# Kernel tuning notes

Measured on AMD Instinct MI355X. Metric: run time of the kernel, lower is better.

The kernel has to match this reference:

```python
import jax, jax.numpy as jnp
import numpy as np

DECAY = 0.99
EPS = 1e-05
B, C, H, W = 64, 64, 64, 64   # C == embedding_dim
K = 512                       # num_embedding


def setup_inputs() -> dict:
    key = jax.random.key(0)
    k1, k2 = jax.random.split(key)
    inp = jax.random.normal(k1, (B, C, H, W), dtype=jnp.float32)
    embedding = jax.random.normal(k2, (C, K), dtype=jnp.float32)
    cluster_size = jnp.zeros((K,), dtype=jnp.float32)
    embedding_avg = embedding  # buffer initialized as a clone of embedding
    return {"input": inp, "embedding": embedding,
            "cluster_size": cluster_size, "embedding_avg": embedding_avg}


def reference(input, embedding, cluster_size, embedding_avg):
    # NCHW -> NHWC, flatten to [N, C]
    x = jnp.transpose(input, (0, 2, 3, 1))           # [B,H,W,C]
    flat = x.reshape(-1, embedding.shape[0])          # [N,C]
    # squared L2 distances to all K codes: [N,K]
    dist = (jnp.sum(flat * flat, axis=1, keepdims=True)
            - 2.0 * flat @ embedding
            + jnp.sum(embedding * embedding, axis=0, keepdims=True))
    ind = jnp.argmin(dist, axis=1)                    # [N] int
    # gather codes (uses OLD embedding, as in torch)
    quantize = jnp.take(embedding.T, ind, axis=0).reshape(x.shape)  # [B,H,W,C]
    # EMA updates (training branch). Avoid materializing one-hot:
    counts = jnp.zeros((K,), dtype=flat.dtype).at[ind].add(1.0)      # onehot.sum(0)
    embedding_sum = jax.ops.segment_sum(flat, ind, num_segments=K).T  # [C,K] == flat.T @ onehot
    new_cluster_size = cluster_size * DECAY + (1.0 - DECAY) * counts
    new_embedding_avg = embedding_avg * DECAY + (1.0 - DECAY) * embedding_sum
    n = jnp.sum(new_cluster_size)
    cs = (new_cluster_size + EPS) / (n + K * EPS) * n
    new_embedding = new_embedding_avg / cs[None, :]
    # commitment loss and straight-through estimator
    diff = jnp.mean((jax.lax.stop_gradient(quantize) - x) ** 2)
    quantize_st = x + jax.lax.stop_gradient(quantize - x)
    out = jnp.transpose(quantize_st, (0, 3, 1, 2))    # back to NCHW
    embedding_ind = ind.reshape(x.shape[:-1])         # [B,H,W]
    return out, diff, embedding_ind, new_embedding, new_cluster_size, new_embedding_avg
```

## Files before the change

### kernel.cpp

```cpp
#include <hip/hip_runtime.h>
#include <cstdint>
#include <cstddef>

typedef _Float16 half4v __attribute__((ext_vector_type(4)));
typedef _Float16 half8v __attribute__((ext_vector_type(8)));
typedef float    f32x4  __attribute__((ext_vector_type(4)));

#define N_PTS   262144
#define CDIM    64
#define KCODES  512
#define TAUA    5e-3f
#define FLAG_CAP 65536u

#define OFF_DIFF 16777216u
#define OFF_IND  16777217u
#define OFF_EMB  17039361u
#define OFF_CSZ  17072129u
#define OFF_AVG  17072641u

__global__ __launch_bounds__(512) void k_main(
    const float* __restrict__ in, const float* __restrict__ emb,
    float* __restrict__ out,
    int* __restrict__ ind_buf, float* __restrict__ diff_acc,
    unsigned* __restrict__ nflag, int* __restrict__ flaglist)
{
    __shared__ __align__(16) char bsm[133120];
    float* ee2_lds = (float*)(bsm + 131072);
    const int tid = threadIdx.x;

    {
        const int col = tid;
        const int xr  = (col & 7) << 4;
        float s = 0.f;
        #pragma unroll
        for (int c0 = 0; c0 < CDIM; c0 += 4) {
            float v[4];
            #pragma unroll
            for (int i = 0; i < 4; ++i) v[i] = emb[(c0 + i)*KCODES + col];
            half4v h, lo;
            #pragma unroll
            for (int i = 0; i < 4; ++i) {
                s = fmaf(v[i], v[i], s);
                _Float16 hh = (_Float16)v[i];
                h[i]  = hh;
                lo[i] = (_Float16)(v[i] - (float)hh);
            }
            const int wb = col*128 + ((c0*2) ^ xr);
            *(half4v*)(bsm + wb)         = h;
            *(half4v*)(bsm + 65536 + wb) = lo;
        }
        ee2_lds[col] = 0.5f * s;
    }
    __syncthreads();

    const int w  = tid >> 6, l = tid & 63;
    const int g  = l >> 4,  lc = l & 15;

    for (int r = 0; r < 2; ++r) {
        const int pbase = (blockIdx.x << 10) + (r << 9) + (w << 6);
        const int b     = pbase >> 12;
        const float* inb = in + ((size_t)b << 18) + ((pbase & 4095) + lc);

        half8v ah[4][2], al[4][2];
        float xs = 0.f;
        #pragma unroll
        for (int t = 0; t < 4; ++t)
            #pragma unroll
            for (int s = 0; s < 2; ++s)
                #pragma unroll
                for (int j = 0; j < 8; ++j) {
                    const int c = s*32 + g*8 + j;
                    const float x = inb[(size_t)c*4096 + t*16];
                    xs = fmaf(x, x, xs);
                    const float xf = -x;
                    const _Float16 hh = (_Float16)xf;
                    ah[t][s][j] = hh;
                    al[t][s][j] = (_Float16)(xf - (float)hh);
                }

        float d1[4][4], d2[4][4]; int k1[4][4];
        #pragma unroll
        for (int t = 0; t < 4; ++t)
            #pragma unroll
            for (int rr = 0; rr < 4; ++rr) { d1[t][rr] = 3.4e38f; d2[t][rr] = 3.4e38f; k1[t][rr] = 0; }

        for (int ct = 0; ct < 32; ++ct) {
            const int col  = (ct << 4) + lc;
            const float sd = ee2_lds[col];
            const int rb   = col*128 + ((g*16) ^ ((col & 7) << 4));
            half8v bh0 = *(const half8v*)(bsm + rb);
            half8v bh1 = *(const half8v*)(bsm + (rb ^ 64));
            half8v bl0 = *(const half8v*)(bsm + 65536 + rb);
            half8v bl1 = *(const half8v*)(bsm + 65536 + (rb ^ 64));

            #pragma unroll
            for (int t = 0; t < 4; ++t) {
                f32x4 acc = {sd, sd, sd, sd};
                acc = __builtin_amdgcn_mfma_f32_16x16x32_f16(al[t][0], bh0, acc, 0, 0, 0);
                acc = __builtin_amdgcn_mfma_f32_16x16x32_f16(al[t][1], bh1, acc, 0, 0, 0);
                acc = __builtin_amdgcn_mfma_f32_16x16x32_f16(ah[t][0], bl0, acc, 0, 0, 0);
                acc = __builtin_amdgcn_mfma_f32_16x16x32_f16(ah[t][1], bl1, acc, 0, 0, 0);
                acc = __builtin_amdgcn_mfma_f32_16x16x32_f16(ah[t][0], bh0, acc, 0, 0, 0);
                acc = __builtin_amdgcn_mfma_f32_16x16x32_f16(ah[t][1], bh1, acc, 0, 0, 0);
                #pragma unroll
                for (int rr = 0; rr < 4; ++rr) {
                    const float d = acc[rr];
                    const bool cc = d < d1[t][rr];
                    d2[t][rr] = fminf(d2[t][rr], fmaxf(d, d1[t][rr]));
                    d1[t][rr] = fminf(d1[t][rr], d);
                    k1[t][rr] = cc ? col : k1[t][rr];
                }
            }
        }

        #pragma unroll
        for (int m = 1; m <= 8; m <<= 1) {
            #pragma unroll
            for (int t = 0; t < 4; ++t)
                #pragma unroll
                for (int rr = 0; rr < 4; ++rr) {
                    const float od1 = __shfl_xor(d1[t][rr], m);
                    const int   ok1 = __shfl_xor(k1[t][rr], m);
                    const float od2 = __shfl_xor(d2[t][rr], m);
                    const float nd2 = fminf(fmaxf(d1[t][rr], od1), fminf(d2[t][rr], od2));
                    const bool take = (od1 < d1[t][rr]) || (od1 == d1[t][rr] && ok1 < k1[t][rr]);
                    d1[t][rr] = take ? od1 : d1[t][rr];
                    k1[t][rr] = take ? ok1 : k1[t][rr];
                    d2[t][rr] = nd2;
                }
        }

        float ds = 0.f;
        if (lc == 0) {
            #pragma unroll
            for (int t = 0; t < 4; ++t) {
                const int nb = pbase + t*16 + (g << 2);
                int4 iv = make_int4(k1[t][0], k1[t][1], k1[t][2], k1[t][3]);
                *(int4*)(ind_buf + nb) = iv;
                #pragma unroll
                for (int rr = 0; rr < 4; ++rr) {
                    out[OFF_IND + nb + rr] = (float)k1[t][rr];
                    ds += d1[t][rr];
                    if (d2[t][rr] - d1[t][rr] < TAUA) {
                        unsigned ix = atomicAdd(nflag, 1u);
                        if (ix < FLAG_CAP) flaglist[ix] = nb + rr;
                    }
                }
            }
        }
        #pragma unroll
        for (int m = 1; m < 64; m <<= 1) {
            ds += __shfl_xor(ds, m);
            xs += __shfl_xor(xs, m);
        }
        if (l == 0) atomicAdd(diff_acc, 2.f*ds + xs);
    }
}

__global__ void k_refine(const float* __restrict__ in, const float* __restrict__ emb,
                         const unsigned* __restrict__ nflag, const int* __restrict__ flaglist,
                         int* __restrict__ ind_buf, float* __restrict__ out)
{
    const int gtid = blockIdx.x*blockDim.x + threadIdx.x;
    const int wid  = gtid >> 6;
    const int lane = threadIdx.x & 63;
    const int nw   = (gridDim.x * blockDim.x) >> 6;
    unsigned nf = *nflag; if (nf > FLAG_CAP) nf = FLAG_CAP;
    for (unsigned f = wid; f < nf; f += nw) {
        const int n = flaglist[f];
        const int b = n >> 12, hw = n & 4095;
        const float* xb = in + ((size_t)b << 18) + hw;
        const float* er = emb + lane*8;
        double dd[8] = {0,0,0,0,0,0,0,0};
        for (int c = 0; c < CDIM; ++c) {
            const double xv = (double)xb[(size_t)c << 12];
            #pragma unroll
            for (int j = 0; j < 8; ++j) {
                double t = xv - (double)er[c*KCODES + j];
                dd[j] = fma(t, t, dd[j]);
            }
        }
        double bd = 1e300; int bk = 0;
        #pragma unroll
        for (int j = 0; j < 8; ++j) {
            const int kk = lane*8 + j;
            if (dd[j] < bd) { bd = dd[j]; bk = kk; }
        }
        for (int off = 32; off; off >>= 1) {
            double od = __shfl_xor(bd, off);
            int    ok = __shfl_xor(bk, off);
            if (od < bd || (od == bd && ok < bk)) { bd = od; bk = ok; }
        }
        if (lane == 0) { ind_buf[n] = bk; out[OFF_IND + n] = (float)bk; }
    }
}

__global__ __launch_bounds__(512) void k_stats(const float* __restrict__ in,
    const int* __restrict__ ind_buf, float* __restrict__ p_sum, float* __restrict__ p_cnt)
{
    __shared__ __align__(16) char xsm[2][CDIM*128];
    __shared__ int   ind_lds[2][32];
    __shared__ float s_cnt[KCODES];

    const int tid = threadIdx.x;
    const int wg  = blockIdx.x;
    const int n0  = wg << 10;
    const int b   = n0 >> 12;
    const float* inb = in + ((size_t)b << 18) + (n0 & 4095);

    for (int i = tid; i < KCODES; i += 512) s_cnt[i] = 0.f;

    const int sc  = tid >> 3;
    const int sp  = (tid & 7) << 2;
    const int sxr = (sc & 7) << 4;
    const int wb_hi = sc*128 + ((sp*2)      ^ sxr);
    const int wb_lo = sc*128 + ((64 + sp*2) ^ sxr);

    const int w  = tid >> 6, l = tid & 63;
    const int g  = l >> 4,  lc = l & 15;
    const int k0w = w << 6;

    f32x4 acc[4][4];
    #pragma unroll
    for (int ci = 0; ci < 4; ++ci)
        #pragma unroll
        for (int kt = 0; kt < 4; ++kt) acc[ci][kt] = (f32x4){0.f, 0.f, 0.f, 0.f};

    {
        const float4 xv = *(const float4*)(inb + (size_t)sc*4096 + sp);
        half4v h, lo;
        #pragma unroll
        for (int i = 0; i < 4; ++i) {
            const float x = ((const float*)&xv)[i];
            _Float16 hh = (_Float16)x;
            h[i] = hh; lo[i] = (_Float16)(x - (float)hh);
        }
        *(half4v*)(&xsm[0][0] + wb_hi) = h;
        *(half4v*)(&xsm[0][0] + wb_lo) = lo;
        if (tid < 8) *(int4*)&ind_lds[0][tid*4] = *(const int4*)(ind_buf + n0 + tid*4);
    }

    for (int t = 0; t < 32; ++t) {
        __syncthreads();
        float4 nxt; int4 niv;
        if (t < 31) {
            nxt = *(const float4*)(inb + (size_t)sc*4096 + (t+1)*32 + sp);
            if (tid < 8) niv = *(const int4*)(ind_buf + n0 + (t+1)*32 + tid*4);
        }
        if (tid < 32) atomicAdd(&s_cnt[ind_lds[t & 1][tid]], 1.f);

        const char* xb = &xsm[t & 1][0];
        half8v ah[4], al[4];
        #pragma unroll
        for (int ci = 0; ci < 4; ++ci) {
            const int c  = (ci << 4) + lc;
            const int xr = (c & 7) << 4;
            ah[ci] = *(const half8v*)(xb + c*128 + ((g*16)      ^ xr));
            al[ci] = *(const half8v*)(xb + c*128 + ((64 + g*16) ^ xr));
        }
        int idv[8];
        *(int4*)&idv[0] = *(const int4*)&ind_lds[t & 1][g*8];
        *(int4*)&idv[4] = *(const int4*)&ind_lds[t & 1][g*8 + 4];
        #pragma unroll
        for (int kt = 0; kt < 4; ++kt) {
            const int tgt = k0w + (kt << 4) + lc;
            half8v bf;
            #pragma unroll
            for (int j = 0; j < 8; ++j) bf[j] = (idv[j] == tgt) ? (_Float16)1.0f : (_Float16)0.0f;
            #pragma unroll
            for (int ci = 0; ci < 4; ++ci) {
                acc[ci][kt] = __builtin_amdgcn_mfma_f32_16x16x32_f16(ah[ci], bf, acc[ci][kt], 0, 0, 0);
                acc[ci][kt] = __builtin_amdgcn_mfma_f32_16x16x32_f16(al[ci], bf, acc[ci][kt], 0, 0, 0);
            }
        }
        if (t < 31) {
            half4v h, lo;
            #pragma unroll
            for (int i = 0; i < 4; ++i) {
                const float x = ((const float*)&nxt)[i];
                _Float16 hh = (_Float16)x;
                h[i] = hh; lo[i] = (_Float16)(x - (float)hh);
            }
            char* xn = &xsm[(t+1) & 1][0];
            *(half4v*)(xn + wb_hi) = h;
            *(half4v*)(xn + wb_lo) = lo;
            if (tid < 8) *(int4*)&ind_lds[(t+1) & 1][tid*4] = niv;
        }
    }
    __syncthreads();

    float* ps = p_sum + (size_t)wg * (CDIM*KCODES);
    #pragma unroll
    for (int ci = 0; ci < 4; ++ci)
        #pragma unroll
        for (int kt = 0; kt < 4; ++kt)
            #pragma unroll
            for (int rr = 0; rr < 4; ++rr)
                ps[((ci << 4) + (g << 2) + rr)*KCODES + k0w + (kt << 4) + lc] = acc[ci][kt][rr];
    float* pc = p_cnt + wg * KCODES;
    for (int i = tid; i < KCODES; i += 512) pc[i] = s_cnt[i];
}

__global__ __launch_bounds__(256) void k_reduce1(const float* __restrict__ p_sum,
    const float* __restrict__ p_cnt, float* __restrict__ partial8,
    float* __restrict__ cnt8, int wsl)
{
    const int ic = blockIdx.x & 31, ws = blockIdx.x >> 5;
    const int i4 = ic*1024 + threadIdx.x*4;
    const float* base = p_sum + (size_t)ws*wsl*(CDIM*KCODES) + i4;
    float4 s = make_float4(0.f, 0.f, 0.f, 0.f);
    for (int w = 0; w < wsl; ++w) {
        const float4 v = *(const float4*)(base + (size_t)w*(CDIM*KCODES));
        s.x += v.x; s.y += v.y; s.z += v.z; s.w += v.w;
    }
    *(float4*)(partial8 + ws*(CDIM*KCODES) + i4) = s;
    if (ic == 0) {
        for (int k = threadIdx.x; k < KCODES; k += 256) {
            float c = 0.f;
            for (int w = 0; w < wsl; ++w) c += p_cnt[(ws*wsl + w)*KCODES + k];
            cnt8[ws*KCODES + k] = c;
        }
    }
}

__global__ __launch_bounds__(256) void k_reduce2(const float* __restrict__ partial8,
    const float* __restrict__ cnt8, float* __restrict__ sum_tot, float* __restrict__ cnt_tot)
{
    const int i4 = (blockIdx.x*256 + threadIdx.x)*4;
    float4 s = make_float4(0.f, 0.f, 0.f, 0.f);
    #pragma unroll
    for (int p = 0; p < 8; ++p) {
        const float4 v = *(const float4*)(partial8 + p*(CDIM*KCODES) + i4);
        s.x += v.x; s.y += v.y; s.z += v.z; s.w += v.w;
    }
    *(float4*)(sum_tot + i4) = s;
    if (blockIdx.x == 0) {
        for (int k = threadIdx.x; k < KCODES; k += 256) {
            float c = 0.f;
            #pragma unroll
            for (int p = 0; p < 8; ++p) c += cnt8[p*KCODES + k];
            cnt_tot[k] = c;
        }
    }
}

__global__ __launch_bounds__(512) void k_scalars(const float* __restrict__ csz,
    const float* __restrict__ cnt_tot, const float* __restrict__ diff_acc,
    float* __restrict__ out, float* __restrict__ cs_ws)
{
    __shared__ float red[512];
    const int k = threadIdx.x;
    const float ncs = csz[k]*0.99f + 0.01f*cnt_tot[k];
    out[OFF_CSZ + k] = ncs;
    red[k] = ncs;
    __syncthreads();
    for (int s = 256; s > 0; s >>= 1) { if (k < s) red[k] += red[k+s]; __syncthreads(); }
    const float n = red[0];
    cs_ws[k] = (ncs + 1e-5f) / (n + 0.00512f) * n;
    if (k == 0) out[OFF_DIFF] = diff_acc[0] * (1.f/16777216.f);
}

__global__ void k_emb(const float* __restrict__ eavg, const float* __restrict__ sum_tot,
                      const float* __restrict__ cs_ws, float* __restrict__ out)
{
    const int i = blockIdx.x*blockDim.x + threadIdx.x;
    const float avg = eavg[i]*0.99f + 0.01f*sum_tot[i];
    out[OFF_AVG + i] = avg;
    out[OFF_EMB + i] = avg / cs_ws[i & (KCODES-1)];
}

__global__ void k_quant(const float* __restrict__ emb, const int* __restrict__ ind_buf,
                        float* __restrict__ out)
{
    const int gid = blockIdx.x*blockDim.x + threadIdx.x;
    const int i  = gid << 2;
    const int hw = i & 4095;
    const int c  = (i >> 12) & 63;
    const int b  = i >> 18;
    const int n  = (b << 12) + hw;
    const int4 iv = *(const int4*)(ind_buf + n);
    const float* er = emb + (c << 9);
    float4 o = make_float4(er[iv.x], er[iv.y], er[iv.z], er[iv.w]);
    *(float4*)(out + i) = o;
}

extern "C" void kernel_launch(void* const* d_in, const int* in_sizes, int n_in,
                              void* d_out, int out_size, void* d_ws, size_t ws_size,
                              hipStream_t stream)
{
    const float* in   = (const float*)d_in[0];
    const float* emb  = (const float*)d_in[1];
    const float* csz  = (const float*)d_in[2];
    const float* eavg = (const float*)d_in[3];
    float* out = (float*)d_out;
    char* ws = (char*)d_ws;

    int*      ind      = (int*)(ws + 2048);
    float*    diff_acc = (float*)(ws + 1050624);
    unsigned* nflag    = (unsigned*)(ws + 1050640);
    int*      flaglist = (int*)(ws + 1050656);
    float*    cs_ws    = (float*)(ws + 1312800);
    float*    cnt_tot  = (float*)(ws + 1314848);
    float*    sum_tot  = (float*)(ws + 1316896);
    const size_t off_part = 1447968;
    const int swgs = 256;
    float* p_sum    = (float*)(ws + off_part);
    float* p_cnt    = (float*)(ws + off_part + (size_t)swgs*(CDIM*KCODES)*4);
    float* partial8 = (float*)(ws + off_part + (size_t)swgs*133120);
    float* cnt8     = (float*)(ws + off_part + (size_t)swgs*133120 + 1048576);

    hipMemsetAsync(ws + 1050624, 0, 32, stream);

    hipLaunchKernelGGL(k_main,    dim3(256),   dim3(512), 0, stream, in, emb, out, ind, diff_acc, nflag, flaglist);
    hipLaunchKernelGGL(k_refine,  dim3(256),   dim3(256), 0, stream, in, emb, nflag, flaglist, ind, out);
    hipLaunchKernelGGL(k_stats,   dim3(256),   dim3(512), 0, stream, in, ind, p_sum, p_cnt);
    hipLaunchKernelGGL(k_reduce1, dim3(256),   dim3(256), 0, stream, p_sum, p_cnt, partial8, cnt8, swgs >> 3);
    hipLaunchKernelGGL(k_reduce2, dim3(32),    dim3(256), 0, stream, partial8, cnt8, sum_tot, cnt_tot);
    hipLaunchKernelGGL(k_scalars, dim3(1),     dim3(512), 0, stream, csz, cnt_tot, diff_acc, out, cs_ws);
    hipLaunchKernelGGL(k_emb,     dim3(128),   dim3(256), 0, stream, eavg, sum_tot, cs_ws, out);
    hipLaunchKernelGGL(k_quant,   dim3(16384), dim3(256), 0, stream, emb, ind, out);
}
```

Before: 217.1 us.

## Stream codebook through half-size LDS in k_main to raise occupancy

k_main no longer holds the whole fp16 hi/lo split codebook in LDS. It now loads and converts the codebook in two 256-code halves per point batch, using 64KB of LDS, and sets launch bounds asking for more resident blocks. Each wave now handles 32 points per pass instead of 64, and the grid doubles to 512 blocks so all points are still covered. The aim is higher occupancy and more parallelism for latency hiding. The cost is repeated codebook loads and conversions (four per block), extra barriers, and less reuse of each LDS B-fragment across point tiles.

```diff
diff --git a/kernel.cpp b/kernel.cpp
--- a/kernel.cpp
+++ b/kernel.cpp
@@ -18,53 +18,38 @@
 #define OFF_CSZ  17072129u
 #define OFF_AVG  17072641u
 
-__global__ __launch_bounds__(512) void k_main(
+__global__ __launch_bounds__(512, 4) void k_main(
     const float* __restrict__ in, const float* __restrict__ emb,
     float* __restrict__ out,
     int* __restrict__ ind_buf, float* __restrict__ diff_acc,
     unsigned* __restrict__ nflag, int* __restrict__ flaglist)
 {
-    __shared__ __align__(16) char bsm[133120];
-    float* ee2_lds = (float*)(bsm + 131072);
+    __shared__ __align__(16) char bsm[65536];
+    __shared__ float ee2_lds[KCODES];
     const int tid = threadIdx.x;
 
     {
-        const int col = tid;
-        const int xr  = (col & 7) << 4;
         float s = 0.f;
         #pragma unroll
-        for (int c0 = 0; c0 < CDIM; c0 += 4) {
-            float v[4];
-            #pragma unroll
-            for (int i = 0; i < 4; ++i) v[i] = emb[(c0 + i)*KCODES + col];
-            half4v h, lo;
-            #pragma unroll
-            for (int i = 0; i < 4; ++i) {
-                s = fmaf(v[i], v[i], s);
-                _Float16 hh = (_Float16)v[i];
-                h[i]  = hh;
-                lo[i] = (_Float16)(v[i] - (float)hh);
-            }
-            const int wb = col*128 + ((c0*2) ^ xr);
-            *(half4v*)(bsm + wb)         = h;
-            *(half4v*)(bsm + 65536 + wb) = lo;
-        }
-        ee2_lds[col] = 0.5f * s;
-    }
-    __syncthreads();
+        for (int c = 0; c < CDIM; ++c) { const float v = emb[c*KCODES + tid]; s = fmaf(v, v, s); }
+        ee2_lds[tid] = 0.5f * s;
+    }
 
     const int w  = tid >> 6, l = tid & 63;
     const int g  = l >> 4,  lc = l & 15;
+    const int scol = tid & 255;
+    const int scs  = (tid >> 8) << 5;
+    const int sxr  = (scol & 7) << 4;
 
     for (int r = 0; r < 2; ++r) {
-        const int pbase = (blockIdx.x << 10) + (r << 9) + (w << 6);
+        const int pbase = (blockIdx.x << 9) + (r << 5) + (w << 6);
         const int b     = pbase >> 12;
         const float* inb = in + ((size_t)b << 18) + ((pbase & 4095) + lc);
 
-        half8v ah[4][2], al[4][2];
+        half8v ah[2][2], al[2][2];
         float xs = 0.f;
         #pragma unroll
-        for (int t = 0; t < 4; ++t)
+        for (int t = 0; t < 2; ++t)
             #pragma unroll
             for (int s = 0; s < 2; ++s)
                 #pragma unroll
@@ -78,45 +63,67 @@
                     al[t][s][j] = (_Float16)(xf - (float)hh);
                 }
 
-        float d1[4][4], d2[4][4]; int k1[4][4];
-        #pragma unroll
-        for (int t = 0; t < 4; ++t)
+        float d1[2][4], d2[2][4]; int k1[2][4];
+        #pragma unroll
+        for (int t = 0; t < 2; ++t)
             #pragma unroll
             for (int rr = 0; rr < 4; ++rr) { d1[t][rr] = 3.4e38f; d2[t][rr] = 3.4e38f; k1[t][rr] = 0; }
 
-        for (int ct = 0; ct < 32; ++ct) {
-            const int col  = (ct << 4) + lc;
-            const float sd = ee2_lds[col];
-            const int rb   = col*128 + ((g*16) ^ ((col & 7) << 4));
-            half8v bh0 = *(const half8v*)(bsm + rb);
-            half8v bh1 = *(const half8v*)(bsm + (rb ^ 64));
-            half8v bl0 = *(const half8v*)(bsm + 65536 + rb);
-            half8v bl1 = *(const half8v*)(bsm + 65536 + (rb ^ 64));
-
-            #pragma unroll
-            for (int t = 0; t < 4; ++t) {
-                f32x4 acc = {sd, sd, sd, sd};
-                acc = __builtin_amdgcn_mfma_f32_16x16x32_f16(al[t][0], bh0, acc, 0, 0, 0);
-                acc = __builtin_amdgcn_mfma_f32_16x16x32_f16(al[t][1], bh1, acc, 0, 0, 0);
-                acc = __builtin_amdgcn_mfma_f32_16x16x32_f16(ah[t][0], bl0, acc, 0, 0, 0);
-                acc = __builtin_amdgcn_mfma_f32_16x16x32_f16(ah[t][1], bl1, acc, 0, 0, 0);
-                acc = __builtin_amdgcn_mfma_f32_16x16x32_f16(ah[t][0], bh0, acc, 0, 0, 0);
-                acc = __builtin_amdgcn_mfma_f32_16x16x32_f16(ah[t][1], bh1, acc, 0, 0, 0);
-                #pragma unroll
-                for (int rr = 0; rr < 4; ++rr) {
-                    const float d = acc[rr];
-                    const bool cc = d < d1[t][rr];
-                    d2[t][rr] = fminf(d2[t][rr], fmaxf(d, d1[t][rr]));
-                    d1[t][rr] = fminf(d1[t][rr], d);
-                    k1[t][rr] = cc ? col : k1[t][rr];
+        for (int kh = 0; kh < 2; ++kh) {
+            __syncthreads();
+            #pragma unroll
+            for (int c0 = 0; c0 < 32; c0 += 4) {
+                float v[4];
+                #pragma unroll
+                for (int i = 0; i < 4; ++i) v[i] = emb[(scs + c0 + i)*KCODES + (kh << 8) + scol];
+                half4v h, lo;
+                #pragma unroll
+                for (int i = 0; i < 4; ++i) {
+                    const _Float16 hh = (_Float16)v[i];
+                    h[i]  = hh;
+                    lo[i] = (_Float16)(v[i] - (float)hh);
                 }
+                const int wb = scol*128 + (((scs + c0)*2) ^ sxr);
+                *(half4v*)(bsm + wb)         = h;
+                *(half4v*)(bsm + 32768 + wb) = lo;
+            }
+            __syncthreads();
+
+            for (int ct = 0; ct < 16; ++ct) {
+                const int col  = (kh << 8) + (ct << 4) + lc;
+                const float sd = ee2_lds[col];
+                const int colh = col & 255;
+                const int rb   = colh*128 + ((g*16) ^ ((colh & 7) << 4));
+                half8v bh0 = *(const half8v*)(bsm + rb);
+                half8v bh1 = *(const half8v*)(bsm + (rb ^ 64));
+                half8v bl0 = *(const half8v*)(bsm + 32768 + rb);
+                half8v bl1 = *(const half8v*)(bsm + 32768 + (rb ^ 64));
+
+                #pragma unroll
+                for (int t = 0; t < 2; ++t) {
+                    f32x4 acc = {sd, sd, sd, sd};
+                    acc = __builtin_amdgcn_mfma_f32_16x16x32_f16(al[t][0], bh0, acc, 0, 0, 0);
+                    acc = __builtin_amdgcn_mfma_f32_16x16x32_f16(al[t][1], bh1, acc, 0, 0, 0);
+                    acc = __builtin_amdgcn_mfma_f32_16x16x32_f16(ah[t][0], bl0, acc, 0, 0, 0);
+                    acc = __builtin_amdgcn_mfma_f32_16x16x32_f16(ah[t][1], bl1, acc, 0, 0, 0);
+                    acc = __builtin_amdgcn_mfma_f32_16x16x32_f16(ah[t][0], bh0, acc, 0, 0, 0);
+                    acc = __builtin_amdgcn_mfma_f32_16x16x32_f16(ah[t][1], bh1, acc, 0, 0, 0);
+                    #pragma unroll
+                    for (int rr = 0; rr < 4; ++rr) {
+                        const float d = acc[rr];
+                        const bool cc = d < d1[t][rr];
+                        d2[t][rr] = fminf(d2[t][rr], fmaxf(d, d1[t][rr]));
+                        d1[t][rr] = fminf(d1[t][rr], d);
+                        k1[t][rr] = cc ? col : k1[t][rr];
+                    }
+                }
             }
         }
 
         #pragma unroll
         for (int m = 1; m <= 8; m <<= 1) {
             #pragma unroll
-            for (int t = 0; t < 4; ++t)
+            for (int t = 0; t < 2; ++t)
                 #pragma unroll
                 for (int rr = 0; rr < 4; ++rr) {
                     const float od1 = __shfl_xor(d1[t][rr], m);
@@ -133,7 +140,7 @@
         float ds = 0.f;
         if (lc == 0) {
             #pragma unroll
-            for (int t = 0; t < 4; ++t) {
+            for (int t = 0; t < 2; ++t) {
                 const int nb = pbase + t*16 + (g << 2);
                 int4 iv = make_int4(k1[t][0], k1[t][1], k1[t][2], k1[t][3]);
                 *(int4*)(ind_buf + nb) = iv;
@@ -411,7 +418,7 @@
 
     hipMemsetAsync(ws + 1050624, 0, 32, stream);
 
-    hipLaunchKernelGGL(k_main,    dim3(256),   dim3(512), 0, stream, in, emb, out, ind, diff_acc, nflag, flaglist);
+    hipLaunchKernelGGL(k_main,    dim3(512),   dim3(512), 0, stream, in, emb, out, ind, diff_acc, nflag, flaglist);
     hipLaunchKernelGGL(k_refine,  dim3(256),   dim3(256), 0, stream, in, emb, nflag, flaglist, ind, out);
     hipLaunchKernelGGL(k_stats,   dim3(256),   dim3(512), 0, stream, in, ind, p_sum, p_cnt);
     hipLaunchKernelGGL(k_reduce1, dim3(256),   dim3(256), 0, stream, p_sum, p_cnt, partial8, cnt8, swgs >> 3);
```

Measured after the change: 270.7 us. 24.7% more time.
